# Performance work log

Measured on AMD Instinct MI355X. Metric: run time of the kernel, lower is better.

The kernel has to match this reference:

```python
import jax, jax.numpy as jnp
import numpy as np
from jax import lax

B, L, D = 2, 4096, 2048
K, KQ, M, H = 32, 4, 8, 8  # H = D*expand // (K*M)
MEM = K * H              # 256
FLAT = K * H * M         # 2048
CONV_W = 4
DIM_SWIGLU = H * 3 * 2   # out_expand_factor=3 -> 48
N_DECAY = K - 4          # 28 decay heads, 4 anchor heads


def setup_inputs() -> dict:
    key = jax.random.key(0)
    ks = jax.random.split(key, 8)
    x = jax.random.normal(ks[0], (B, L, D), dtype=jnp.float32)
    W_mem = jax.random.normal(ks[1], (D, MEM + K), dtype=jnp.float32) / np.sqrt(D)
    conv_k = jax.random.normal(ks[2], (CONV_W, 1, MEM + K), dtype=jnp.float32) * 0.3
    W_q = jax.random.normal(ks[3], (D, KQ * H * M * 2), dtype=jnp.float32) / np.sqrt(D)
    theta = jnp.asarray(np.tile(np.geomspace(0.001, 3.0, M).reshape(1, 1, 1, 1, M),
                                (1, 1, K, H, 1)), dtype=jnp.float32)
    decay_slopes = jnp.asarray(np.log(np.expm1(np.geomspace(0.001, 0.1, N_DECAY))), dtype=jnp.float32)
    anchor_slopes = jnp.asarray(np.log(np.expm1(np.geomspace(0.01, 0.1, 4))), dtype=jnp.float32)
    score_scale = jnp.ones((K,), dtype=jnp.float32)
    g = np.sqrt(2.0 / (H + DIM_SWIGLU))
    W_re = jax.random.normal(ks[4], (K, H, DIM_SWIGLU), dtype=jnp.float32) * g
    W_im = jax.random.normal(ks[5], (K, H, DIM_SWIGLU), dtype=jnp.float32) * g
    norm_scale = jnp.ones((1, 1, K, H), dtype=jnp.float32)
    W_out = jax.random.normal(ks[6], (K * H * 3, D), dtype=jnp.float32) / np.sqrt(K * H * 3)
    return {"x": x, "W_mem": W_mem, "conv_k": conv_k, "W_q": W_q, "theta": theta,
            "decay_slopes": decay_slopes, "anchor_slopes": anchor_slopes,
            "score_scale": score_scale, "W_re": W_re, "W_im": W_im,
            "norm_scale": norm_scale, "W_out": W_out}


def _forward(x, W_mem, conv_k, W_q, theta, decay_slopes, anchor_slopes,
             score_scale, W_re, W_im, norm_scale, W_out):
    b, l, d = x.shape
    # memory branch: dense + causal depthwise conv
    z = x @ W_mem  # (b, l, MEM+K)
    z = lax.conv_general_dilated(z, conv_k, window_strides=(1,),
                                 padding=[(CONV_W - 1, 0)],
                                 dimension_numbers=('NHC', 'HIO', 'NHC'),
                                 feature_group_count=MEM + K)
    k_val = z[..., :MEM].reshape(b, l, K, H)
    s_raw = z[..., MEM:].reshape(b, l, K, 1)
    # query branch
    q = (x @ W_q).reshape(b, l, KQ, H, M, 2)
    q_re, q_im = q[..., 0], q[..., 1]
    # per-head time weights (decay heads look back from end, anchor heads from start)
    pos = jnp.arange(l, dtype=jnp.float32)
    slopes_d = jax.nn.softplus(decay_slopes).reshape(1, 1, -1, 1)
    slopes_a = jax.nn.softplus(anchor_slopes).reshape(1, 1, -1, 1)
    dist = jnp.maximum(jnp.float32(l - 1) - pos, 0.0)
    log_w = jnp.concatenate([-slopes_d * dist[None, :, None, None],
                             -slopes_a * pos[None, :, None, None]], axis=2)  # (1,l,K,1)
    log_p = jnp.clip(score_scale[None, None, :, None] * s_raw, -20.0, 20.0)
    p_w = jnp.exp(log_p + log_w)  # (b,l,K,1)
    # complex rotation of keys
    phi = k_val[..., None] * theta          # (b,l,K,H,M)
    re_k, im_k = jnp.cos(phi), jnp.sin(phi)
    pw5 = p_w[..., None]
    merged = jnp.concatenate([p_w.squeeze(-1),
                              (pw5 * re_k).reshape(b, l, FLAT),
                              (pw5 * im_k).reshape(b, l, FLAT)], axis=-1)
    cs = jnp.cumsum(merged, axis=1)
    den = cs[..., :K]                       # (b,l,K)
    num_re = cs[..., K:K + FLAT]
    num_im = cs[..., K + FLAT:]
    inv_den = 1.0 / jnp.maximum(den[..., None], 1e-4)  # (b,l,K,1)
    state_re = num_re.reshape(b, l, K, H, M) * inv_den[..., None]
    state_im = num_im.reshape(b, l, K, H, M) * inv_den[..., None]
    # GQA-style query repeat
    n_rep = K // KQ
    q_re = jnp.repeat(q_re, n_rep, axis=2)
    q_im = jnp.repeat(q_im, n_rep, axis=2)
    out_re = jnp.sum(state_re * q_re + state_im * q_im, axis=-1)  # (b,l,K,H)
    out_im = jnp.sum(state_im * q_re - state_re * q_im, axis=-1)
    out_re = out_re * norm_scale
    out_im = out_im * norm_scale
    y = jnp.einsum('blkh,khn->blkn', out_re, W_re) + jnp.einsum('blkh,khn->blkn', out_im, W_im)
    y_val, y_gate = jnp.split(y, 2, axis=-1)
    y = (y_val * jax.nn.silu(y_gate)).reshape(b, l, -1)
    return y @ W_out


def reference(x, W_mem, conv_k, W_q, theta, decay_slopes, anchor_slopes,
              score_scale, W_re, W_im, norm_scale, W_out):
    return _forward(x, W_mem, conv_k, W_q, theta, decay_slopes, anchor_slopes,
                    score_scale, W_re, W_im, norm_scale, W_out)
```

## Files before the change

kernel.cpp:

```cpp
#include <hip/hip_runtime.h>
#include <hip/hip_bf16.h>
#include <math.h>

#define BB 2
#define LL 4096
#define DD 2048
#define KK 32
#define MEM 256
#define CTOT 288
#define NQ 512
#define ZSTR 800
#define NPAD 896
#define FLAT 2048
#define CMERG 4128
#define CH 16
#define NCH 256
#define YDIM 768
#define KV2 1536
#define BL (BB*LL)

typedef __attribute__((ext_vector_type(4))) float f32x4;
typedef __attribute__((ext_vector_type(8))) short bf16x8;
typedef __attribute__((ext_vector_type(8))) unsigned short u16x8;

__device__ inline unsigned short f2b(float v) {
    __hip_bfloat16 h = __float2bfloat16(v);
    return *reinterpret_cast<unsigned short*>(&h);
}
__device__ inline float b2f(unsigned short u) {
    __hip_bfloat16 h;
    *reinterpret_cast<unsigned short*>(&h) = u;
    return __bfloat162float(h);
}

__device__ inline void gload16(const void* g, void* l) {
    __builtin_amdgcn_global_load_lds(
        (const __attribute__((address_space(1))) unsigned int*)g,
        (__attribute__((address_space(3))) unsigned int*)l, 16, 0, 0);
}

template<int HH>
__device__ inline float bcast8(float v) {
    return __int_as_float(__builtin_amdgcn_ds_swizzle(__float_as_int(v), (HH << 5) | 0x18));
}

__device__ inline float fast_sigmoid_mul(float val, float g) {
    return val * __builtin_amdgcn_rcpf(1.f + __expf(-g));
}

__global__ __launch_bounds__(256) void cvt_x(const float* __restrict__ x,
                                             unsigned short* __restrict__ xb) {
    size_t i = ((size_t)blockIdx.x * 256 + threadIdx.x) * 8;
    float4 a = *(const float4*)&x[i];
    float4 b = *(const float4*)&x[i + 4];
    u16x8 o;
    o[0] = f2b(a.x); o[1] = f2b(a.y); o[2] = f2b(a.z); o[3] = f2b(a.w);
    o[4] = f2b(b.x); o[5] = f2b(b.y); o[6] = f2b(b.z); o[7] = f2b(b.w);
    *(u16x8*)&xb[i] = o;
}

__global__ __launch_bounds__(256) void prep_wb(const float* __restrict__ W_mem,
                                               const float* __restrict__ W_q,
                                               unsigned short* __restrict__ Wb) {
    int n = blockIdx.x;
    for (int k = threadIdx.x; k < DD; k += 256) {
        float v = 0.f;
        if (n < CTOT) v = W_mem[(size_t)k * CTOT + n];
        else if (n < ZSTR) v = W_q[(size_t)k * NQ + (n - CTOT)];
        Wb[(size_t)n * DD + k] = f2b(v);
    }
}

__global__ __launch_bounds__(256) void prep_wo(const float* __restrict__ W_out,
                                               unsigned short* __restrict__ Wo) {
    int n = blockIdx.x;
    for (int k = threadIdx.x; k < YDIM; k += 256) {
        float v = W_out[(size_t)k * DD + n];
        unsigned short hi = f2b(v);
        float r = v - b2f(hi);
        Wo[(size_t)n * KV2 + k] = hi;
        Wo[(size_t)n * KV2 + YDIM + k] = f2b(r);
    }
}

template<bool CBF16>
__global__ __launch_bounds__(256) void gemm_mfma(const unsigned short* __restrict__ A,
                                                 const unsigned short* __restrict__ Bh_g,
                                                 void* __restrict__ Cout,
                                                 int Kd, int Nvalid, int Cstride) {
    __shared__ unsigned short As[2][4096];
    __shared__ unsigned short Bh[2][4096];
    int tid = threadIdx.x;
    int lane = tid & 63;
    int wave = tid >> 6;
    int wr = wave >> 1, wc = wave & 1;

    int nwg = gridDim.x * gridDim.y;
    int bid = blockIdx.y * gridDim.x + blockIdx.x;
    int cpx = nwg >> 3;
    int swz = (bid & 7) * cpx + (bid >> 3);
    int bx = swz % gridDim.x, by = swz / gridDim.x;
    int m0 = by * 128;
    int n0 = bx * 128;

    f32x4 acc[4][4];
#pragma unroll
    for (int i = 0; i < 4; ++i)
#pragma unroll
        for (int j = 0; j < 4; ++j) acc[i][j] = (f32x4){0.f, 0.f, 0.f, 0.f};

    int f0 = tid, f1 = 256 + tid;
    int row0 = f0 >> 2, ks0 = (f0 & 3) ^ ((row0 >> 1) & 3);
    int row1 = f1 >> 2, ks1 = (f1 & 3) ^ ((row1 >> 1) & 3);
    const unsigned short* ga0 = &A[(size_t)(m0 + row0) * Kd + ks0 * 8];
    const unsigned short* ga1 = &A[(size_t)(m0 + row1) * Kd + ks1 * 8];
    const unsigned short* gb0 = &Bh_g[(size_t)(n0 + row0) * Kd + ks0 * 8];
    const unsigned short* gb1 = &Bh_g[(size_t)(n0 + row1) * Kd + ks1 * 8];
    int l0 = (wave * 64) * 8;
    int l1 = (256 + wave * 64) * 8;

    int g = lane >> 4, rr = lane & 15;

#define STAGE(buf, koff) do {                                          \
        gload16(ga0 + (koff), &As[buf][l0]);                           \
        gload16(ga1 + (koff), &As[buf][l1]);                           \
        gload16(gb0 + (koff), &Bh[buf][l0]);                           \
        gload16(gb1 + (koff), &Bh[buf][l1]);                           \
    } while (0)

    STAGE(0, 0);
    __syncthreads();

    int nIter = Kd >> 5;
    int cur = 0;
    for (int it = 0; it < nIter; ++it) {
        if (it + 1 < nIter) STAGE(cur ^ 1, (it + 1) * 32);

        bf16x8 av[4], bhv[4];
#pragma unroll
        for (int i = 0; i < 4; ++i) {
            int ra = wr * 64 + i * 16 + rr;
            av[i] = *(const bf16x8*)&As[cur][ra * 32 + ((g ^ ((ra >> 1) & 3)) * 8)];
            int rb = wc * 64 + i * 16 + rr;
            bhv[i] = *(const bf16x8*)&Bh[cur][rb * 32 + ((g ^ ((rb >> 1) & 3)) * 8)];
        }
#pragma unroll
        for (int i = 0; i < 4; ++i)
#pragma unroll
            for (int j = 0; j < 4; ++j)
                acc[i][j] = __builtin_amdgcn_mfma_f32_16x16x32_bf16(av[i], bhv[j], acc[i][j], 0, 0, 0);

        __syncthreads();
        cur ^= 1;
    }
#undef STAGE

    int cg = lane >> 4, cr = lane & 15;
#pragma unroll
    for (int i = 0; i < 4; ++i)
#pragma unroll
        for (int j = 0; j < 4; ++j) {
            int colb = n0 + wc * 64 + j * 16 + cr;
            if (colb < Nvalid) {
#pragma unroll
                for (int r = 0; r < 4; ++r) {
                    int rowb = m0 + wr * 64 + i * 16 + cg * 4 + r;
                    if (CBF16)
                        ((unsigned short*)Cout)[(size_t)rowb * Cstride + colb] = f2b(acc[i][j][r]);
                    else
                        ((float*)Cout)[(size_t)rowb * Cstride + colb] = acc[i][j][r];
                }
            }
        }
}

__global__ __launch_bounds__(512, 2) void gemm256(const unsigned short* __restrict__ A,
                                                  const unsigned short* __restrict__ Bm,
                                                  float* __restrict__ C,
                                                  int KA, int Kv, int Cstride) {
    __shared__ __attribute__((aligned(16))) unsigned short As[2][16384];
    __shared__ __attribute__((aligned(16))) unsigned short Bs[2][16384];
    int tid = threadIdx.x;
    int lane = tid & 63, wave = tid >> 6;
    int wm = wave >> 2, wn = wave & 3;

    int nwg = gridDim.x * gridDim.y;
    int bid = blockIdx.y * gridDim.x + blockIdx.x;
    int cpx = nwg >> 3;
    int swz = (bid & 7) * cpx + (bid >> 3);
    int bx = swz % gridDim.x, by = swz / gridDim.x;
    int m0 = by * 256, n0 = bx * 256;

    f32x4 acc[8][4];
#pragma unroll
    for (int i = 0; i < 8; ++i)
#pragma unroll
        for (int j = 0; j < 4; ++j) acc[i][j] = (f32x4){0.f, 0.f, 0.f, 0.f};

    const unsigned short* pA[4];
    const unsigned short* pB[4];
    int ldsoff[4];
#pragma unroll
    for (int j = 0; j < 4; ++j) {
        int f = j * 512 + tid;
        int row = f >> 3, s = f & 7;
        int sg = s ^ (row & 7);
        pA[j] = A + (size_t)(m0 + row) * KA + sg * 8;
        pB[j] = Bm + (size_t)(n0 + row) * Kv + sg * 8;
        ldsoff[j] = (j * 512 + wave * 64) * 8;
    }

    int rr = lane & 15, kg = lane >> 4;

    gload16(pB[0], &Bs[0][ldsoff[0]]); gload16(pB[1], &Bs[0][ldsoff[1]]);
    gload16(pB[2], &Bs[0][ldsoff[2]]); gload16(pB[3], &Bs[0][ldsoff[3]]);
    gload16(pA[0], &As[0][ldsoff[0]]); gload16(pA[2], &As[0][ldsoff[2]]);
    gload16(pA[1], &As[0][ldsoff[1]]); gload16(pA[3], &As[0][ldsoff[3]]);
    asm volatile("s_waitcnt vmcnt(2)" ::: "memory");
    __builtin_amdgcn_s_barrier();

    int nT = Kv >> 6;
    int cur = 0;

#define LDA(fr, t) ({ int ra_ = wm * 128 + (fr) * 16 + rr;                       \
        int sd_ = (t) * 4 + kg;                                                  \
        *(const bf16x8*)&As[cur][(ra_ * 8 + (sd_ ^ (ra_ & 7))) * 8]; })
#define LDB(fc, t) ({ int rb_ = wn * 64 + (fc) * 16 + rr;                        \
        int sd_ = (t) * 4 + kg;                                                  \
        *(const bf16x8*)&Bs[cur][(rb_ * 8 + (sd_ ^ (rb_ & 7))) * 8]; })

#define MFMA16(io) do {                                                           \
    __builtin_amdgcn_s_setprio(1);                                                \
    _Pragma("unroll")                                                             \
    for (int i = 0; i < 4; ++i)                                                   \
        _Pragma("unroll")                                                         \
        for (int j = 0; j < 4; ++j)                                               \
            acc[(io) + i][j] = __builtin_amdgcn_mfma_f32_16x16x32_bf16(av[i], bv[j], acc[(io) + i][j], 0, 0, 0); \
    __builtin_amdgcn_s_setprio(0);                                                \
} while (0)

    for (int it = 0; it < nT; ++it) {
        int nxt = cur ^ 1;
        bool hn = (it + 1 < nT);
        int k0n = (it + 1) << 6;
        int kkA = (k0n >= KA) ? (k0n - KA) : k0n;
        bf16x8 av[4], bv[4];

#pragma unroll
        for (int j = 0; j < 4; ++j) bv[j] = LDB(j, 0);
#pragma unroll
        for (int j = 0; j < 4; ++j) av[j] = LDA(j, 0);
        if (hn) { gload16(pB[0] + k0n, &Bs[nxt][ldsoff[0]]); gload16(pB[1] + k0n, &Bs[nxt][ldsoff[1]]); }
        __builtin_amdgcn_s_barrier();
        MFMA16(0);
        __builtin_amdgcn_s_barrier();

#pragma unroll
        for (int j = 0; j < 4; ++j) bv[j] = LDB(j, 1);
#pragma unroll
        for (int j = 0; j < 4; ++j) av[j] = LDA(j, 1);
        if (hn) {
            gload16(pB[2] + k0n, &Bs[nxt][ldsoff[2]]); gload16(pB[3] + k0n, &Bs[nxt][ldsoff[3]]);
            asm volatile("s_waitcnt vmcnt(4)" ::: "memory");
        } else {
            asm volatile("s_waitcnt vmcnt(0)" ::: "memory");
        }
        __builtin_amdgcn_s_barrier();
        MFMA16(0);
        __builtin_amdgcn_s_barrier();

#pragma unroll
        for (int j = 0; j < 4; ++j) bv[j] = LDB(j, 0);
#pragma unroll
        for (int j = 0; j < 4; ++j) av[j] = LDA(4 + j, 0);
        if (hn) { gload16(pA[0] + kkA, &As[nxt][ldsoff[0]]); gload16(pA[2] + kkA, &As[nxt][ldsoff[2]]); }
        __builtin_amdgcn_s_barrier();
        MFMA16(4);
        __builtin_amdgcn_s_barrier();

#pragma unroll
        for (int j = 0; j < 4; ++j) bv[j] = LDB(j, 1);
#pragma unroll
        for (int j = 0; j < 4; ++j) av[j] = LDA(4 + j, 1);
        if (hn) {
            gload16(pA[1] + kkA, &As[nxt][ldsoff[1]]); gload16(pA[3] + kkA, &As[nxt][ldsoff[3]]);
            asm volatile("s_waitcnt vmcnt(2)" ::: "memory");
        }
        __builtin_amdgcn_s_barrier();
        MFMA16(4);
        __builtin_amdgcn_s_barrier();

        cur = nxt;
    }
#undef LDA
#undef LDB
#undef MFMA16

#pragma unroll
    for (int i = 0; i < 8; ++i)
#pragma unroll
        for (int j = 0; j < 4; ++j) {
            int colb = n0 + wn * 64 + j * 16 + rr;
#pragma unroll
            for (int r = 0; r < 4; ++r) {
                int rowb = m0 + wm * 128 + i * 16 + kg * 4 + r;
                C[(size_t)rowb * Cstride + colb] = acc[i][j][r];
            }
        }
}

__global__ __launch_bounds__(256) void fused_partial(const unsigned short* __restrict__ zq,
                                                     const float* __restrict__ conv_k,
                                                     const float* __restrict__ theta,
                                                     const float* __restrict__ decay,
                                                     const float* __restrict__ anchor,
                                                     const float* __restrict__ sscale,
                                                     float* __restrict__ partials) {
    int chunk = blockIdx.x, b = blockIdx.y, t = threadIdx.x;
    int l0 = chunk * CH;
    __shared__ unsigned short zin[CH + 3][CTOT];

    for (int idx = t; idx < (CH + 3) * 36; idx += 256) {
        int r = idx / 36, c8 = (idx % 36) * 8;
        int l = l0 - 3 + r;
        u16x8 v = (u16x8)(0);
        if (l >= 0) v = *(const u16x8*)&zq[(size_t)(b * LL + l) * ZSTR + c8];
        *(u16x8*)&zin[r][c8] = v;
    }
    __syncthreads();

    int k = t >> 3;
    float cz0 = conv_k[t], cz1 = conv_k[CTOT + t], cz2 = conv_k[2 * CTOT + t], cz3 = conv_k[3 * CTOT + t];
    int sc = MEM + k;
    float cs0 = conv_k[sc], cs1 = conv_k[CTOT + sc], cs2 = conv_k[2 * CTOT + sc], cs3 = conv_k[3 * CTOT + sc];
    float xx = (k < KK - 4) ? decay[k] : anchor[k - (KK - 4)];
    float sp = (xx > 20.f) ? xx : log1pf(__expf(xx));
    float ss = sscale[k];
    float th[8];
#pragma unroll
    for (int m = 0; m < 8; ++m) th[m] = theta[t * 8 + m];
    float rs[8], is[8];
#pragma unroll
    for (int m = 0; m < 8; ++m) { rs[m] = 0.f; is[m] = 0.f; }
    float dsum = 0.f;

#pragma unroll 1
    for (int i = 0; i < CH; ++i) {
        float kv = b2f(zin[i][t]) * cz0 + b2f(zin[i + 1][t]) * cz1 +
                   b2f(zin[i + 2][t]) * cz2 + b2f(zin[i + 3][t]) * cz3;
        float s = b2f(zin[i][sc]) * cs0 + b2f(zin[i + 1][sc]) * cs1 +
                  b2f(zin[i + 2][sc]) * cs2 + b2f(zin[i + 3][sc]) * cs3;
        int l = l0 + i;
        float lw = (k < KK - 4) ? -sp * (float)(LL - 1 - l) : -sp * (float)l;
        float lp = fminf(fmaxf(ss * s, -20.f), 20.f);
        float p = __expf(lp + lw);
        dsum += p;
#pragma unroll
        for (int m = 0; m < 8; ++m) {
            float sn, cn;
            __sincosf(kv * th[m], &sn, &cn);
            rs[m] += p * cn;
            is[m] += p * sn;
        }
    }
    size_t base = ((size_t)b * NCH + chunk) * CMERG;
    *(f32x4*)&partials[base + KK + t * 8]            = (f32x4){rs[0], rs[1], rs[2], rs[3]};
    *(f32x4*)&partials[base + KK + t * 8 + 4]        = (f32x4){rs[4], rs[5], rs[6], rs[7]};
    *(f32x4*)&partials[base + KK + FLAT + t * 8]     = (f32x4){is[0], is[1], is[2], is[3]};
    *(f32x4*)&partials[base + KK + FLAT + t * 8 + 4] = (f32x4){is[4], is[5], is[6], is[7]};
    if ((t & 7) == 0) partials[base + k] = dsum;
}

__global__ __launch_bounds__(256) void scan_partials(float* __restrict__ partials) {
    int t = threadIdx.x;
    int cl = t & 15, j = t >> 4;
    int c = blockIdx.x * 16 + cl;
    int b = blockIdx.y;
    float v[16];
    float s = 0.f;
#pragma unroll
    for (int i = 0; i < 16; ++i) {
        v[i] = partials[((size_t)b * NCH + j * 16 + i) * CMERG + c];
        s += v[i];
    }
    __shared__ float sums[16][17];
    sums[j][cl] = s;
    __syncthreads();
    if (j == 0) {
        float run = 0.f;
#pragma unroll
        for (int jj = 0; jj < 16; ++jj) {
            float x = sums[jj][cl];
            sums[jj][cl] = run;
            run += x;
        }
    }
    __syncthreads();
    float run = sums[j][cl];
#pragma unroll
    for (int i = 0; i < 16; ++i) {
        float x = v[i];
        partials[((size_t)b * NCH + j * 16 + i) * CMERG + c] = run;
        run += x;
    }
}

__global__ __launch_bounds__(256) void fused_stage(const unsigned short* __restrict__ zq,
                                                   const float* __restrict__ conv_k,
                                                   const float* __restrict__ theta,
                                                   const float* __restrict__ decay,
                                                   const float* __restrict__ anchor,
                                                   const float* __restrict__ sscale,
                                                   const float* __restrict__ partials,
                                                   const float* __restrict__ W_re,
                                                   const float* __restrict__ W_im,
                                                   const float* __restrict__ nscale,
                                                   unsigned short* __restrict__ y_act) {
    int chunk = blockIdx.x, b = blockIdx.y, t = threadIdx.x;
    int l0 = chunk * CH;
    __shared__ unsigned short zin[CH + 3][CTOT];
    __shared__ unsigned short qall[CH][NQ];

    for (int idx = t; idx < (CH + 3) * 36; idx += 256) {
        int r = idx / 36, c8 = (idx % 36) * 8;
        int l = l0 - 3 + r;
        u16x8 v = (u16x8)(0);
        if (l >= 0) v = *(const u16x8*)&zq[(size_t)(b * LL + l) * ZSTR + c8];
        *(u16x8*)&zin[r][c8] = v;
    }
    for (int idx = t; idx < CH * (NQ / 8); idx += 256) {
        int i = idx >> 6, c8 = (idx & 63) * 8;
        *(u16x8*)&qall[i][c8] = *(const u16x8*)&zq[(size_t)(b * LL + l0 + i) * ZSTR + CTOT + c8];
    }
    __syncthreads();

    int k = t >> 3, h = t & 7, w = t >> 6;
    float cz0 = conv_k[t], cz1 = conv_k[CTOT + t], cz2 = conv_k[2 * CTOT + t], cz3 = conv_k[3 * CTOT + t];
    int sc = MEM + k;
    float cs0 = conv_k[sc], cs1 = conv_k[CTOT + sc], cs2 = conv_k[2 * CTOT + sc], cs3 = conv_k[3 * CTOT + sc];
    float xx = (k < KK - 4) ? decay[k] : anchor[k - (KK - 4)];
    float sp = (xx > 20.f) ? xx : log1pf(__expf(xx));
    float ss = sscale[k];
    float th[8];
#pragma unroll
    for (int m = 0; m < 8; ++m) th[m] = theta[t * 8 + m];
    float ns = nscale[t];
    int qb = w * 128 + h * 16;

    float wre[8][6], wim[8][6];
#pragma unroll
    for (int hh = 0; hh < 8; ++hh)
#pragma unroll
        for (int jj = 0; jj < 6; ++jj) {
            wre[hh][jj] = W_re[(k * 8 + hh) * 48 + h + 8 * jj];
            wim[hh][jj] = W_im[(k * 8 + hh) * 48 + h + 8 * jj];
        }

    size_t pbase = ((size_t)b * NCH + chunk) * CMERG;
    f32x4 r0 = *(const f32x4*)&partials[pbase + KK + t * 8];
    f32x4 r1 = *(const f32x4*)&partials[pbase + KK + t * 8 + 4];
    f32x4 i0 = *(const f32x4*)&partials[pbase + KK + FLAT + t * 8];
    f32x4 i1 = *(const f32x4*)&partials[pbase + KK + FLAT + t * 8 + 4];
    float rs[8] = {r0[0], r0[1], r0[2], r0[3], r1[0], r1[1], r1[2], r1[3]};
    float is[8] = {i0[0], i0[1], i0[2], i0[3], i1[0], i1[1], i1[2], i1[3]};
    float den = partials[pbase + k];

#pragma unroll 1
    for (int i = 0; i < CH; ++i) {
        float kv = b2f(zin[i][t]) * cz0 + b2f(zin[i + 1][t]) * cz1 +
                   b2f(zin[i + 2][t]) * cz2 + b2f(zin[i + 3][t]) * cz3;
        float s = b2f(zin[i][sc]) * cs0 + b2f(zin[i + 1][sc]) * cs1 +
                  b2f(zin[i + 2][sc]) * cs2 + b2f(zin[i + 3][sc]) * cs3;
        int l = l0 + i;
        float lw = (k < KK - 4) ? -sp * (float)(LL - 1 - l) : -sp * (float)l;
        float lp = fminf(fmaxf(ss * s, -20.f), 20.f);
        float p = __expf(lp + lw);
        den += p;
        float inv = __builtin_amdgcn_rcpf(fmaxf(den, 1e-4f));
#pragma unroll
        for (int m = 0; m < 8; ++m) {
            float sn, cn;
            __sincosf(kv * th[m], &sn, &cn);
            rs[m] += p * cn;
            is[m] += p * sn;
        }
        u16x8 qv0 = *(const u16x8*)&qall[i][qb];
        u16x8 qv1 = *(const u16x8*)&qall[i][qb + 8];
        float o_re = 0.f, o_im = 0.f;
#pragma unroll
        for (int m = 0; m < 8; ++m) {
            float sre = rs[m] * inv;
            float sim = is[m] * inv;
            float qre = b2f((unsigned short)((m < 4) ? qv0[2 * m] : qv1[2 * m - 8]));
            float qim = b2f((unsigned short)((m < 4) ? qv0[2 * m + 1] : qv1[2 * m - 7]));
            o_re += sre * qre + sim * qim;
            o_im += sim * qre - sre * qim;
        }
        o_re *= ns;
        o_im *= ns;

        float y0 = 0.f, y1 = 0.f, y2 = 0.f, y3 = 0.f, y4 = 0.f, y5 = 0.f;
#define EAPPLY(HH) { float br_ = bcast8<HH>(o_re); float bi_ = bcast8<HH>(o_im); \
        y0 += br_ * wre[HH][0] + bi_ * wim[HH][0]; \
        y1 += br_ * wre[HH][1] + bi_ * wim[HH][1]; \
        y2 += br_ * wre[HH][2] + bi_ * wim[HH][2]; \
        y3 += br_ * wre[HH][3] + bi_ * wim[HH][3]; \
        y4 += br_ * wre[HH][4] + bi_ * wim[HH][4]; \
        y5 += br_ * wre[HH][5] + bi_ * wim[HH][5]; }
        EAPPLY(0) EAPPLY(1) EAPPLY(2) EAPPLY(3)
        EAPPLY(4) EAPPLY(5) EAPPLY(6) EAPPLY(7)
#undef EAPPLY

        size_t ybase = (size_t)(b * LL + l) * YDIM + k * 24 + h;
        y_act[ybase]      = f2b(fast_sigmoid_mul(y0 * y3, y3));
        y_act[ybase + 8]  = f2b(fast_sigmoid_mul(y1 * y4, y4));
        y_act[ybase + 16] = f2b(fast_sigmoid_mul(y2 * y5, y5));
    }
}

extern "C" void kernel_launch(void* const* d_in, const int* in_sizes, int n_in,
                              void* d_out, int out_size, void* d_ws, size_t ws_size,
                              hipStream_t stream) {
    const float* x      = (const float*)d_in[0];
    const float* W_mem  = (const float*)d_in[1];
    const float* conv_k = (const float*)d_in[2];
    const float* W_q    = (const float*)d_in[3];
    const float* theta  = (const float*)d_in[4];
    const float* decay  = (const float*)d_in[5];
    const float* anchor = (const float*)d_in[6];
    const float* sscale = (const float*)d_in[7];
    const float* W_re   = (const float*)d_in[8];
    const float* W_im   = (const float*)d_in[9];
    const float* nscale = (const float*)d_in[10];
    const float* W_out  = (const float*)d_in[11];
    float* out = (float*)d_out;
    float* ws = (float*)d_ws;

    unsigned short* xb = (unsigned short*)out;
    unsigned short* Wb = (unsigned short*)(out + 8388608);
    unsigned short* zq = (unsigned short*)(out + 9306112);
    float* partials      = ws;
    unsigned short* yb   = (unsigned short*)(ws + 2113536);
    unsigned short* Wo   = (unsigned short*)(ws + 5259264);

    cvt_x<<<8192, 256, 0, stream>>>(x, xb);
    prep_wb<<<NPAD, 256, 0, stream>>>(W_mem, W_q, Wb);
    prep_wo<<<DD, 256, 0, stream>>>(W_out, Wo);

    gemm_mfma<true><<<dim3(NPAD / 128, BL / 128), 256, 0, stream>>>(
        xb, Wb, zq, DD, ZSTR, ZSTR);
    fused_partial<<<dim3(NCH, BB), 256, 0, stream>>>(zq, conv_k, theta, decay, anchor, sscale, partials);
    scan_partials<<<dim3(CMERG / 16, BB), 256, 0, stream>>>(partials);
    fused_stage<<<dim3(NCH, BB), 256, 0, stream>>>(zq, conv_k, theta, decay, anchor, sscale,
                                                   partials, W_re, W_im, nscale, yb);
    gemm256<<<dim3(DD / 256, BL / 256), 512, 0, stream>>>(yb, Wo, out, YDIM, KV2, DD);
}
```

Before: 180.4 us.

## Switch gemm256 to 32x32x16 bf16 MFMA with four-phase K loop

Rewrites the 256x256 GEMM inner loop to use 32x32x16 MFMA instructions instead of 16x16x32, with each wave holding 4x2 f32x16 accumulators. The K tile is processed in four sub-steps, each issuing a few next-tile global-to-LDS loads spread across phases, followed by 8 MFMAs. The intent is fewer LDS fragment reads per MFMA and higher MFMA throughput per instruction. In exchange it waits on all outstanding loads (vmcnt(0)) at the end of each tile instead of the earlier partial waits, and changes the epilogue store pattern.

```diff
diff --git a/kernel.cpp b/kernel.cpp
--- a/kernel.cpp
+++ b/kernel.cpp
@@ -20,6 +20,7 @@
 #define BL (BB*LL)
 
 typedef __attribute__((ext_vector_type(4))) float f32x4;
+typedef __attribute__((ext_vector_type(16))) float f32x16;
 typedef __attribute__((ext_vector_type(8))) short bf16x8;
 typedef __attribute__((ext_vector_type(8))) unsigned short u16x8;
 
@@ -191,11 +192,13 @@
     int bx = swz % gridDim.x, by = swz / gridDim.x;
     int m0 = by * 256, n0 = bx * 256;
 
-    f32x4 acc[8][4];
-#pragma unroll
-    for (int i = 0; i < 8; ++i)
-#pragma unroll
-        for (int j = 0; j < 4; ++j) acc[i][j] = (f32x4){0.f, 0.f, 0.f, 0.f};
+    f32x16 acc[4][2];
+#pragma unroll
+    for (int i = 0; i < 4; ++i)
+#pragma unroll
+        for (int j = 0; j < 2; ++j)
+#pragma unroll
+            for (int r = 0; r < 16; ++r) acc[i][j][r] = 0.f;
 
     const unsigned short* pA[4];
     const unsigned short* pB[4];
@@ -210,100 +213,77 @@
         ldsoff[j] = (j * 512 + wave * 64) * 8;
     }
 
-    int rr = lane & 15, kg = lane >> 4;
-
-    gload16(pB[0], &Bs[0][ldsoff[0]]); gload16(pB[1], &Bs[0][ldsoff[1]]);
-    gload16(pB[2], &Bs[0][ldsoff[2]]); gload16(pB[3], &Bs[0][ldsoff[3]]);
-    gload16(pA[0], &As[0][ldsoff[0]]); gload16(pA[2], &As[0][ldsoff[2]]);
-    gload16(pA[1], &As[0][ldsoff[1]]); gload16(pA[3], &As[0][ldsoff[3]]);
-    asm volatile("s_waitcnt vmcnt(2)" ::: "memory");
+    int l31 = lane & 31, l5 = lane >> 5;
+
+#pragma unroll
+    for (int j = 0; j < 4; ++j) gload16(pB[j], &Bs[0][ldsoff[j]]);
+#pragma unroll
+    for (int j = 0; j < 4; ++j) gload16(pA[j], &As[0][ldsoff[j]]);
+    asm volatile("s_waitcnt vmcnt(0)" ::: "memory");
     __builtin_amdgcn_s_barrier();
 
     int nT = Kv >> 6;
     int cur = 0;
 
-#define LDA(fr, t) ({ int ra_ = wm * 128 + (fr) * 16 + rr;                       \
-        int sd_ = (t) * 4 + kg;                                                  \
+#define LDA32(rb, t) ({ int ra_ = wm * 128 + (rb) * 32 + l31;                    \
+        int sd_ = (t) * 2 + l5;                                                  \
         *(const bf16x8*)&As[cur][(ra_ * 8 + (sd_ ^ (ra_ & 7))) * 8]; })
-#define LDB(fc, t) ({ int rb_ = wn * 64 + (fc) * 16 + rr;                        \
-        int sd_ = (t) * 4 + kg;                                                  \
+#define LDB32(cb, t) ({ int rb_ = wn * 64 + (cb) * 32 + l31;                     \
+        int sd_ = (t) * 2 + l5;                                                  \
         *(const bf16x8*)&Bs[cur][(rb_ * 8 + (sd_ ^ (rb_ & 7))) * 8]; })
-
-#define MFMA16(io) do {                                                           \
-    __builtin_amdgcn_s_setprio(1);                                                \
-    _Pragma("unroll")                                                             \
-    for (int i = 0; i < 4; ++i)                                                   \
-        _Pragma("unroll")                                                         \
-        for (int j = 0; j < 4; ++j)                                               \
-            acc[(io) + i][j] = __builtin_amdgcn_mfma_f32_16x16x32_bf16(av[i], bv[j], acc[(io) + i][j], 0, 0, 0); \
-    __builtin_amdgcn_s_setprio(0);                                                \
-} while (0)
 
     for (int it = 0; it < nT; ++it) {
         int nxt = cur ^ 1;
         bool hn = (it + 1 < nT);
         int k0n = (it + 1) << 6;
         int kkA = (k0n >= KA) ? (k0n - KA) : k0n;
-        bf16x8 av[4], bv[4];
-
-#pragma unroll
-        for (int j = 0; j < 4; ++j) bv[j] = LDB(j, 0);
-#pragma unroll
-        for (int j = 0; j < 4; ++j) av[j] = LDA(j, 0);
-        if (hn) { gload16(pB[0] + k0n, &Bs[nxt][ldsoff[0]]); gload16(pB[1] + k0n, &Bs[nxt][ldsoff[1]]); }
-        __builtin_amdgcn_s_barrier();
-        MFMA16(0);
-        __builtin_amdgcn_s_barrier();
-
-#pragma unroll
-        for (int j = 0; j < 4; ++j) bv[j] = LDB(j, 1);
-#pragma unroll
-        for (int j = 0; j < 4; ++j) av[j] = LDA(j, 1);
-        if (hn) {
-            gload16(pB[2] + k0n, &Bs[nxt][ldsoff[2]]); gload16(pB[3] + k0n, &Bs[nxt][ldsoff[3]]);
-            asm volatile("s_waitcnt vmcnt(4)" ::: "memory");
-        } else {
-            asm volatile("s_waitcnt vmcnt(0)" ::: "memory");
-        }
-        __builtin_amdgcn_s_barrier();
-        MFMA16(0);
-        __builtin_amdgcn_s_barrier();
-
-#pragma unroll
-        for (int j = 0; j < 4; ++j) bv[j] = LDB(j, 0);
-#pragma unroll
-        for (int j = 0; j < 4; ++j) av[j] = LDA(4 + j, 0);
-        if (hn) { gload16(pA[0] + kkA, &As[nxt][ldsoff[0]]); gload16(pA[2] + kkA, &As[nxt][ldsoff[2]]); }
-        __builtin_amdgcn_s_barrier();
-        MFMA16(4);
-        __builtin_amdgcn_s_barrier();
-
-#pragma unroll
-        for (int j = 0; j < 4; ++j) bv[j] = LDB(j, 1);
-#pragma unroll
-        for (int j = 0; j < 4; ++j) av[j] = LDA(4 + j, 1);
-        if (hn) {
-            gload16(pA[1] + kkA, &As[nxt][ldsoff[1]]); gload16(pA[3] + kkA, &As[nxt][ldsoff[3]]);
-            asm volatile("s_waitcnt vmcnt(2)" ::: "memory");
-        }
-        __builtin_amdgcn_s_barrier();
-        MFMA16(4);
-        __builtin_amdgcn_s_barrier();
-
+
+#pragma unroll
+        for (int t = 0; t < 4; ++t) {
+            bf16x8 a0 = LDA32(0, t), a1 = LDA32(1, t), a2 = LDA32(2, t), a3 = LDA32(3, t);
+            bf16x8 b0 = LDB32(0, t), b1 = LDB32(1, t);
+            if (hn) {
+                if (t == 0) {
+                    gload16(pB[0] + k0n, &Bs[nxt][ldsoff[0]]);
+                    gload16(pB[1] + k0n, &Bs[nxt][ldsoff[1]]);
+                    gload16(pB[2] + k0n, &Bs[nxt][ldsoff[2]]);
+                } else if (t == 1) {
+                    gload16(pB[3] + k0n, &Bs[nxt][ldsoff[3]]);
+                    gload16(pA[0] + kkA, &As[nxt][ldsoff[0]]);
+                    gload16(pA[1] + kkA, &As[nxt][ldsoff[1]]);
+                } else if (t == 2) {
+                    gload16(pA[2] + kkA, &As[nxt][ldsoff[2]]);
+                    gload16(pA[3] + kkA, &As[nxt][ldsoff[3]]);
+                }
+            }
+            __builtin_amdgcn_s_barrier();
+            __builtin_amdgcn_s_setprio(1);
+            acc[0][0] = __builtin_amdgcn_mfma_f32_32x32x16_bf16(a0, b0, acc[0][0], 0, 0, 0);
+            acc[0][1] = __builtin_amdgcn_mfma_f32_32x32x16_bf16(a0, b1, acc[0][1], 0, 0, 0);
+            acc[1][0] = __builtin_amdgcn_mfma_f32_32x32x16_bf16(a1, b0, acc[1][0], 0, 0, 0);
+            acc[1][1] = __builtin_amdgcn_mfma_f32_32x32x16_bf16(a1, b1, acc[1][1], 0, 0, 0);
+            acc[2][0] = __builtin_amdgcn_mfma_f32_32x32x16_bf16(a2, b0, acc[2][0], 0, 0, 0);
+            acc[2][1] = __builtin_amdgcn_mfma_f32_32x32x16_bf16(a2, b1, acc[2][1], 0, 0, 0);
+            acc[3][0] = __builtin_amdgcn_mfma_f32_32x32x16_bf16(a3, b0, acc[3][0], 0, 0, 0);
+            acc[3][1] = __builtin_amdgcn_mfma_f32_32x32x16_bf16(a3, b1, acc[3][1], 0, 0, 0);
+            __builtin_amdgcn_s_setprio(0);
+            if (t == 3) asm volatile("s_waitcnt vmcnt(0)" ::: "memory");
+            __builtin_amdgcn_s_barrier();
+        }
         cur = nxt;
     }
-#undef LDA
-#undef LDB
-#undef MFMA16
-
-#pragma unroll
-    for (int i = 0; i < 8; ++i)
-#pragma unroll
-        for (int j = 0; j < 4; ++j) {
-            int colb = n0 + wn * 64 + j * 16 + rr;
-#pragma unroll
-            for (int r = 0; r < 4; ++r) {
-                int rowb = m0 + wm * 128 + i * 16 + kg * 4 + r;
+#undef LDA32
+#undef LDB32
+
+#pragma unroll
+    for (int i = 0; i < 4; ++i)
+#pragma unroll
+        for (int j = 0; j < 2; ++j) {
+            int colb = n0 + wn * 64 + j * 32 + l31;
+            int rowb0 = m0 + wm * 128 + i * 32 + 4 * l5;
+#pragma unroll
+            for (int r = 0; r < 16; ++r) {
+                int rowb = rowb0 + (r & 3) + 8 * (r >> 2);
                 C[(size_t)rowb * Cstride + colb] = acc[i][j][r];
             }
         }
```

New measurement: 182.6 us. Within noise of the previous version (+1.2%).

## Simplify GEMM main loop to one-barrier double-buffered schedule

Applied to the files above, without the earlier changes.

Replaces the four-phase interleaved GEMM loop, which had eight barriers per K-tile, with a simpler schedule. All next-tile global-to-LDS loads are issued at the top, then every fragment is read from LDS and the full 8x4 MFMA block runs, then one vmcnt(0) wait and barrier close the tile. This is meant to cut barrier and priority-switch overhead. In exchange it loses the fine-grained overlap of loads with MFMA phases and raises register pressure by holding eight B fragments at once.

```diff
diff --git a/kernel.cpp b/kernel.cpp
--- a/kernel.cpp
+++ b/kernel.cpp
@@ -212,11 +212,11 @@
 
     int rr = lane & 15, kg = lane >> 4;
 
-    gload16(pB[0], &Bs[0][ldsoff[0]]); gload16(pB[1], &Bs[0][ldsoff[1]]);
-    gload16(pB[2], &Bs[0][ldsoff[2]]); gload16(pB[3], &Bs[0][ldsoff[3]]);
-    gload16(pA[0], &As[0][ldsoff[0]]); gload16(pA[2], &As[0][ldsoff[2]]);
-    gload16(pA[1], &As[0][ldsoff[1]]); gload16(pA[3], &As[0][ldsoff[3]]);
-    asm volatile("s_waitcnt vmcnt(2)" ::: "memory");
+#pragma unroll
+    for (int j = 0; j < 4; ++j) gload16(pB[j], &Bs[0][ldsoff[j]]);
+#pragma unroll
+    for (int j = 0; j < 4; ++j) gload16(pA[j], &As[0][ldsoff[j]]);
+    asm volatile("s_waitcnt vmcnt(0)" ::: "memory");
     __builtin_amdgcn_s_barrier();
 
     int nT = Kv >> 6;
@@ -229,73 +229,41 @@
         int sd_ = (t) * 4 + kg;                                                  \
         *(const bf16x8*)&Bs[cur][(rb_ * 8 + (sd_ ^ (rb_ & 7))) * 8]; })
 
-#define MFMA16(io) do {                                                           \
-    __builtin_amdgcn_s_setprio(1);                                                \
-    _Pragma("unroll")                                                             \
-    for (int i = 0; i < 4; ++i)                                                   \
-        _Pragma("unroll")                                                         \
-        for (int j = 0; j < 4; ++j)                                               \
-            acc[(io) + i][j] = __builtin_amdgcn_mfma_f32_16x16x32_bf16(av[i], bv[j], acc[(io) + i][j], 0, 0, 0); \
-    __builtin_amdgcn_s_setprio(0);                                                \
-} while (0)
-
     for (int it = 0; it < nT; ++it) {
         int nxt = cur ^ 1;
         bool hn = (it + 1 < nT);
         int k0n = (it + 1) << 6;
         int kkA = (k0n >= KA) ? (k0n - KA) : k0n;
-        bf16x8 av[4], bv[4];
-
-#pragma unroll
-        for (int j = 0; j < 4; ++j) bv[j] = LDB(j, 0);
-#pragma unroll
-        for (int j = 0; j < 4; ++j) av[j] = LDA(j, 0);
-        if (hn) { gload16(pB[0] + k0n, &Bs[nxt][ldsoff[0]]); gload16(pB[1] + k0n, &Bs[nxt][ldsoff[1]]); }
+
+        if (hn) {
+#pragma unroll
+            for (int j = 0; j < 4; ++j) gload16(pB[j] + k0n, &Bs[nxt][ldsoff[j]]);
+#pragma unroll
+            for (int j = 0; j < 4; ++j) gload16(pA[j] + kkA, &As[nxt][ldsoff[j]]);
+        }
+
+        bf16x8 bv[8];
+#pragma unroll
+        for (int j = 0; j < 4; ++j) { bv[2 * j] = LDB(j, 0); bv[2 * j + 1] = LDB(j, 1); }
+#pragma unroll
+        for (int i = 0; i < 8; ++i) {
+            bf16x8 a0 = LDA(i, 0);
+            bf16x8 a1 = LDA(i, 1);
+#pragma unroll
+            for (int j = 0; j < 4; ++j) {
+                acc[i][j] = __builtin_amdgcn_mfma_f32_16x16x32_bf16(a0, bv[2 * j], acc[i][j], 0, 0, 0);
+                acc[i][j] = __builtin_amdgcn_mfma_f32_16x16x32_bf16(a1, bv[2 * j + 1], acc[i][j], 0, 0, 0);
+            }
+        }
+
+        asm volatile("s_waitcnt vmcnt(0)" ::: "memory");
         __builtin_amdgcn_s_barrier();
-        MFMA16(0);
-        __builtin_amdgcn_s_barrier();
-
-#pragma unroll
-        for (int j = 0; j < 4; ++j) bv[j] = LDB(j, 1);
-#pragma unroll
-        for (int j = 0; j < 4; ++j) av[j] = LDA(j, 1);
-        if (hn) {
-            gload16(pB[2] + k0n, &Bs[nxt][ldsoff[2]]); gload16(pB[3] + k0n, &Bs[nxt][ldsoff[3]]);
-            asm volatile("s_waitcnt vmcnt(4)" ::: "memory");
-        } else {
-            asm volatile("s_waitcnt vmcnt(0)" ::: "memory");
-        }
-        __builtin_amdgcn_s_barrier();
-        MFMA16(0);
-        __builtin_amdgcn_s_barrier();
-
-#pragma unroll
-        for (int j = 0; j < 4; ++j) bv[j] = LDB(j, 0);
-#pragma unroll
-        for (int j = 0; j < 4; ++j) av[j] = LDA(4 + j, 0);
-        if (hn) { gload16(pA[0] + kkA, &As[nxt][ldsoff[0]]); gload16(pA[2] + kkA, &As[nxt][ldsoff[2]]); }
-        __builtin_amdgcn_s_barrier();
-        MFMA16(4);
-        __builtin_amdgcn_s_barrier();
-
-#pragma unroll
-        for (int j = 0; j < 4; ++j) bv[j] = LDB(j, 1);
-#pragma unroll
-        for (int j = 0; j < 4; ++j) av[j] = LDA(4 + j, 1);
-        if (hn) {
-            gload16(pA[1] + kkA, &As[nxt][ldsoff[1]]); gload16(pA[3] + kkA, &As[nxt][ldsoff[3]]);
-            asm volatile("s_waitcnt vmcnt(2)" ::: "memory");
-        }
-        __builtin_amdgcn_s_barrier();
-        MFMA16(4);
-        __builtin_amdgcn_s_barrier();
-
         cur = nxt;
     }
 #undef LDA
 #undef LDB
-#undef MFMA16
-
+
+    int cg = lane >> 4;
 #pragma unroll
     for (int i = 0; i < 8; ++i)
 #pragma unroll
@@ -303,7 +271,7 @@
             int colb = n0 + wn * 64 + j * 16 + rr;
 #pragma unroll
             for (int r = 0; r < 4; ++r) {
-                int rowb = m0 + wm * 128 + i * 16 + kg * 4 + r;
+                int rowb = m0 + wm * 128 + i * 16 + cg * 4 + r;
                 C[(size_t)rowb * Cstride + colb] = acc[i][j][r];
             }
         }
```

After: 183.1 us. About the same (+1.5%).
